# Kernel tuning notes

Measured on AMD Instinct MI355X. Metric: run time of the kernel, lower is better.

The kernel has to match this reference:

```python
import jax, jax.numpy as jnp
import numpy as np

B, H, VOCAB, STEPS = 256, 512, 100, 200  # TEXT_MAX_LEN - 1 = 200
SOS_IDX = 0  # char2idx['<SOS>'] == 0 (first entry of chars list)


def setup_inputs() -> dict:
    key = jax.random.key(0)
    ks = jax.random.split(key, 8)
    s = 0.05  # keep gates/tanh away from saturation, like trained-weight scale
    return {
        "feat": jax.random.normal(ks[0], (B, H), jnp.float32),          # resnet pooler_output
        "embed_table": jax.random.normal(ks[1], (VOCAB, H), jnp.float32) * s,
        "w_ih": jax.random.normal(ks[2], (3 * H, H), jnp.float32) * s,   # torch weight_ih_l0
        "w_hh": jax.random.normal(ks[3], (3 * H, H), jnp.float32) * s,   # torch weight_hh_l0
        "b_ih": jax.random.normal(ks[4], (3 * H,), jnp.float32) * s,
        "b_hh": jax.random.normal(ks[5], (3 * H,), jnp.float32) * s,
        "proj_w": jax.random.normal(ks[6], (VOCAB, H), jnp.float32) * s,
        "proj_b": jax.random.normal(ks[7], (VOCAB,), jnp.float32) * s,
    }


def _gru_cell(x, h, w_ih, w_hh, b_ih, b_hh):
    # torch GRU cell: gates ordered [r, z, n]
    gi = x @ w_ih.T + b_ih          # [B, 3H]
    gh = h @ w_hh.T + b_hh          # [B, 3H]
    i_r, i_z, i_n = jnp.split(gi, 3, axis=-1)
    h_r, h_z, h_n = jnp.split(gh, 3, axis=-1)
    r = jax.nn.sigmoid(i_r + h_r)
    z = jax.nn.sigmoid(i_z + h_z)
    n = jnp.tanh(i_n + r * h_n)
    return (1.0 - z) * n + z * h


def reference(feat, embed_table, w_ih, w_hh, b_ih, b_hh, proj_w, proj_b):
    batch = feat.shape[0]
    # hidden initialized from resnet features; first input = embed(<SOS>)
    h0 = feat                                             # [B, H]
    inp0 = jnp.broadcast_to(embed_table[SOS_IDX], (batch, H))

    def step(carry, _):
        inp, h = carry
        h_new = _gru_cell(inp, h, w_ih, w_hh, b_ih, b_hh)
        # GRU output == new hidden (1 layer); it is fed back as next input
        return (h_new, h_new), h_new

    _, outs = jax.lax.scan(step, (inp0, h0), None, length=STEPS)  # [T, B, H]
    res = jnp.transpose(outs, (1, 0, 2))                          # [B, T, H]
    logits = res @ proj_w.T + proj_b                              # [B, T, V]
    return jnp.transpose(logits, (0, 2, 1))                       # [B, V, T]
```

## Files before the change

### kernel.cpp

```cpp
#include <hip/hip_runtime.h>
#include <hip/hip_bf16.h>
#include <math.h>


typedef __bf16 bf16_t;
typedef __bf16 bf16x8 __attribute__((ext_vector_type(8)));
typedef float f32x4 __attribute__((ext_vector_type(4)));
typedef unsigned long long u64;
typedef unsigned short u16;

#define B_ 256
#define H_ 512
#define V_ 100
#define T_ 200
#define NF_ 131072
#define SLAB_ 24576
#define MFMA(a,b,c) __builtin_amdgcn_mfma_f32_16x16x32_bf16((a),(b),(c),0,0,0)

__device__ __forceinline__ float ld_in(const void* p, long i, int isf32) {
    return isf32 ? ((const float*)p)[i] : (float)((const bf16_t*)p)[i];
}

__device__ __forceinline__ bf16_t split_pick(double v, int sp) {
    bf16_t a = (bf16_t)(float)v;
    if (sp == 0) return a;
    double r1 = v - (double)(float)a;
    bf16_t b = (bf16_t)(float)r1;
    if (sp == 1) return b;
    double r2 = r1 - (double)(float)b;
    return (bf16_t)(float)r2;
}

union bfbits { __bf16 b; u16 u; };

__global__ __launch_bounds__(256) void convert_kernel(
    const void* __restrict__ feat, const void* __restrict__ embed,
    const void* __restrict__ wih,  const void* __restrict__ whh,
    const void* __restrict__ bih,  const void* __restrict__ bhh,
    const void* __restrict__ pw,   const void* __restrict__ pb,
    char* __restrict__ barr, int* __restrict__ flag,
    bf16_t* __restrict__ WB, bf16_t* __restrict__ W0, bf16_t* __restrict__ PB,
    bf16_t* __restrict__ hsp, double* __restrict__ hf,
    double* __restrict__ BB, double* __restrict__ pbd, double* __restrict__ gi0)
{
    __shared__ int s_cnt;
    if (threadIdx.x == 0) s_cnt = 0;
    __syncthreads();
    if (threadIdx.x < 128) {
        unsigned w = ((const unsigned*)feat)[threadIdx.x];
        unsigned e = (w >> 7) & 0xFFu;
        if (e >= 0x68u && e <= 0x85u) atomicAdd(&s_cnt, 1);
    }
    __syncthreads();
    const int isf32 = (s_cnt < 96) ? 1 : 0;
    if (blockIdx.x == 0) {
        if (threadIdx.x == 0) *flag = isf32;
        if (threadIdx.x < 48) {
            int i = threadIdx.x;
            int* p;
            if (i < 32)      p = (int*)(barr + (size_t)i * 128);
            else if (i < 40) p = (int*)(barr + 4096 + (size_t)(i - 32) * 128);
            else             p = (int*)(barr + 8192 + (size_t)(i - 40) * 128);
            *p = 0;
        }
    }

    const long S0 = NF_;
    const long S1 = 3145728;
    const long S2 = 2359296;
    const long S3 = 114688;
    const long S4 = 2048;
    const long S5 = 100;
    const long S6 = 1536;
    const long TOT = S0 + S1 + S2 + S3 + S4 + S5 + S6;

    for (long g = blockIdx.x * 256L + threadIdx.x; g < TOT;
         g += (long)gridDim.x * 256L) {
        long i = g;
        if (i < S0) {
            double v = (double)ld_in(feat, i, isf32);
            hf[i] = v;
            hsp[i] = split_pick(v, 0);
            hsp[NF_ + i] = split_pick(v, 1);
            hsp[2 * NF_ + i] = split_pick(v, 2);
            continue;
        }
        i -= S0;
        if (i < S1) {
            long slab = i / SLAB_;  long rem = i % SLAB_;
            int grp = (int)(slab >> 5), jt = (int)(slab & 31);
            int sp = (int)(rem / 8192); long r2 = rem % 8192;
            int c = (int)(r2 / 512), r = (int)((r2 % 512) / 32), kk = (int)(r2 & 31);
            long n = jt * 16 + r, k = c * 32 + kk;
            double v;
            if (grp == 0)      v = (double)ld_in(wih, n * H_ + k, isf32) +
                                   (double)ld_in(whh, n * H_ + k, isf32);
            else if (grp == 1) v = (double)ld_in(wih, (512 + n) * H_ + k, isf32) +
                                   (double)ld_in(whh, (512 + n) * H_ + k, isf32);
            else if (grp == 2) v = (double)ld_in(wih, (1024 + n) * H_ + k, isf32);
            else               v = (double)ld_in(whh, (1024 + n) * H_ + k, isf32);
            WB[i] = split_pick(v, sp);
            continue;
        }
        i -= S1;
        if (i < S2) {
            long slab = i / SLAB_;  long rem = i % SLAB_;
            int grp = (int)(slab >> 5), jt = (int)(slab & 31);
            int sp = (int)(rem / 8192); long r2 = rem % 8192;
            int c = (int)(r2 / 512), r = (int)((r2 % 512) / 32), kk = (int)(r2 & 31);
            long n = jt * 16 + r, k = c * 32 + kk;
            long row = (grp == 0) ? n : (grp == 1) ? (512 + n) : (1024 + n);
            W0[i] = split_pick((double)ld_in(whh, row * H_ + k, isf32), sp);
            continue;
        }
        i -= S2;
        if (i < S3) {
            int vt = (int)(i / 16384); long rem = i % 16384;
            int sp = (int)(rem / 8192); long r2 = rem % 8192;
            int c = (int)(r2 / 512), r = (int)((r2 % 512) / 32), kk = (int)(r2 & 31);
            int v = vt * 16 + r;
            long k = c * 32 + kk;
            double val = (v < V_) ? (double)ld_in(pw, (long)v * H_ + k, isf32) : 0.0;
            PB[i] = split_pick(val, sp);
            continue;
        }
        i -= S3;
        if (i < S4) {
            int grp = (int)(i / 512), j = (int)(i & 511);
            double v;
            if (grp == 0)      v = (double)ld_in(bih, j, isf32) + (double)ld_in(bhh, j, isf32);
            else if (grp == 1) v = (double)ld_in(bih, 512 + j, isf32) + (double)ld_in(bhh, 512 + j, isf32);
            else if (grp == 2) v = (double)ld_in(bih, 1024 + j, isf32);
            else               v = (double)ld_in(bhh, 1024 + j, isf32);
            BB[i] = v;
            continue;
        }
        i -= S4;
        if (i < S5) { pbd[i] = (double)ld_in(pb, i, isf32); continue; }
        i -= S5;
        if (i < S6) {
            double acc = 0.0;
            #pragma unroll 8
            for (int k = 0; k < H_; ++k)
                acc += (double)ld_in(embed, k, isf32) *
                       (double)ld_in(wih, i * H_ + k, isf32);
            gi0[i] = acc;
        }
    }
}

__global__ __launch_bounds__(512, 2) void gru_persist(
    const bf16_t* __restrict__ WB, const bf16_t* __restrict__ W0,
    const bf16_t* __restrict__ PB,
    bf16_t* __restrict__ hsp,
    const double* __restrict__ hf,
    const double* __restrict__ BB, const double* __restrict__ pbd,
    const double* __restrict__ gi0,
    const int* __restrict__ flag, char* __restrict__ barr,
    void* __restrict__ outp)
{
    __shared__ __align__(16) u64 Ad[2][3072];
    __shared__ double Gm[8][32][16];
    __shared__ __align__(16) bf16_t PBl[16384];

    const int tid = threadIdx.x;
    const int w = tid >> 6;
    const int g = w & 3;
    const int par = w >> 2;
    const int lane = tid & 63;
    const int ln = lane & 15;
    const int quad = lane >> 4;
    const int b = blockIdx.x;
    const int x = b & 7;
    const int l = b >> 3;
    const int jt = (x & 3) * 8 + (l & 7);
    const int mh = (x >> 2) * 4 + (l >> 3);
    const int m0base = mh * 32;
    const int isf32 = *flag;

    int* mysub = (int*)(barr + (size_t)(mh * 4 + (jt >> 3)) * 128);
    int* mytop = (int*)(barr + 4096 + (size_t)mh * 128);
    int* mys   = (int*)(barr + 8192 + (size_t)mh * 128);

    const int gm = tid >> 4;
    const int gj = tid & 15;
    const int jg = jt * 16 + gj;
    double hreg = hf[(long)(m0base + gm) * H_ + jg];
    const double bbR = BB[jg], bbZ = BB[512 + jg];
    const double bbNI = BB[1024 + jg], bbNH = BB[1536 + jg];
    const double g0R = gi0[jg], g0Z = gi0[512 + jg], g0NI = gi0[1024 + jg];

    bf16x8 Breg[8][3];
    {
        const int gg = (g == 3) ? 2 : g;
        const bf16_t* wpre = W0 + (long)(gg * 32 + jt) * SLAB_ + ln * 32 + quad * 8;
        #pragma unroll
        for (int n = 0; n < 8; ++n)
            #pragma unroll
            for (int sp = 0; sp < 3; ++sp)
                Breg[n][sp] = *(const bf16x8*)(wpre + sp * 8192 + (par + 2 * n) * 512);
    }
    const bf16_t* wpW = WB + (long)(g * 32 + jt) * SLAB_ + ln * 32 + quad * 8;

    const int tpj = jt & 1;

    if (jt < 14) {
        const bf16_t* src = PB + (long)(jt >> 1) * 16384;
        #pragma unroll
        for (int it = 0; it < 4; ++it) {
            int cg = it * 512 + tid;
            int h01 = cg >> 10, c = (cg >> 6) & 15, j = cg & 63;
            int L = (j & 3) * 16 + (j >> 2);
            *(bf16x8*)(PBl + h01 * 8192 + c * 512 + L * 8) =
                *(const bf16x8*)(src + cg * 8);
        }
    }

    const int lf = (((ln ^ quad) ^ ((ln & 1) << 2)) | (quad << 4)) * 8;

    int soff[6]; int ldst[6];
    #pragma unroll
    for (int i = 0; i < 6; ++i) {
        int u = i * 512 + tid;
        int sp = u >> 10, row = (u >> 5) & 31, k64 = u & 31;
        soff[i] = sp * 32768 + (m0base + row) * 128 + k64;
        int lc = k64 >> 3, qd = (k64 & 7) >> 1, half = k64 & 1;
        int lpos = (((row & 15) ^ qd) ^ ((row & 1) << 2)) | (qd << 4);
        ldst[i] = sp * 1024 + lc * 256 + (row >> 4) * 128 + lpos * 2 + half;
    }
    __syncthreads();

    for (int s = 0; s <= T_; ++s) {
        const u64* hin64 = (const u64*)(hsp + (long)(s & 1) * 3 * NF_);
        const bool gemm = (s < T_) && !(s == 0 && g == 2);
        const bool doproj = (s >= 1 && jt < 14 && w == (s & 7));

        double dg0[4] = {0, 0, 0, 0}, dg1[4] = {0, 0, 0, 0};
        f32x4 pacc = {0.f, 0.f, 0.f, 0.f};

        u64 sreg[24];
        #pragma unroll
        for (int qq = 0; qq < 4; ++qq)
            #pragma unroll
            for (int i = 0; i < 6; ++i)
                sreg[qq * 6 + i] = __hip_atomic_load(
                    hin64 + (long)soff[i] + qq * 32,
                    __ATOMIC_RELAXED, __HIP_MEMORY_SCOPE_AGENT);

        #pragma unroll
        for (int i = 0; i < 6; ++i) Ad[0][ldst[i]] = sreg[i];
        __syncthreads();

        #pragma unroll
        for (int q = 0; q < 4; ++q) {
            if (q < 3) {
                #pragma unroll
                for (int i = 0; i < 6; ++i)
                    Ad[(q + 1) & 1][ldst[i]] = sreg[(q + 1) * 6 + i];
            }
            const __bf16* Ab = (const __bf16*)(Ad[q & 1]);

            if (gemm) {
                #pragma unroll
                for (int t = 0; t < 2; ++t) {
                    const int lc = 2 * t + par;
                    const int n = 2 * q + t;
                    bf16x8 A0[3], A1[3];
                    #pragma unroll
                    for (int sp = 0; sp < 3; ++sp) {
                        A0[sp] = *(const bf16x8*)(Ab + sp * 4096 + lc * 1024 + lf);
                        A1[sp] = *(const bf16x8*)(Ab + sp * 4096 + lc * 1024 + 512 + lf);
                    }
                    f32x4 t0 = {0.f, 0.f, 0.f, 0.f};
                    t0 = MFMA(A0[0], Breg[n][2], t0);
                    t0 = MFMA(A0[1], Breg[n][1], t0);
                    t0 = MFMA(A0[2], Breg[n][0], t0);
                    t0 = MFMA(A0[0], Breg[n][1], t0);
                    t0 = MFMA(A0[1], Breg[n][0], t0);
                    t0 = MFMA(A0[0], Breg[n][0], t0);
                    f32x4 t1 = {0.f, 0.f, 0.f, 0.f};
                    t1 = MFMA(A1[0], Breg[n][2], t1);
                    t1 = MFMA(A1[1], Breg[n][1], t1);
                    t1 = MFMA(A1[2], Breg[n][0], t1);
                    t1 = MFMA(A1[0], Breg[n][1], t1);
                    t1 = MFMA(A1[1], Breg[n][0], t1);
                    t1 = MFMA(A1[0], Breg[n][0], t1);
                    #pragma unroll
                    for (int i = 0; i < 4; ++i) {
                        dg0[i] += (double)t0[i];
                        dg1[i] += (double)t1[i];
                    }
                }
            }
            if (doproj) {
                #pragma unroll
                for (int lc = 0; lc < 4; ++lc) {
                    const int c = q * 4 + lc;
                    bf16x8 pa1 = *(const bf16x8*)(Ab + 0 * 4096 + lc * 1024 + tpj * 512 + lf);
                    bf16x8 pa2 = *(const bf16x8*)(Ab + 1 * 4096 + lc * 1024 + tpj * 512 + lf);
                    bf16x8 b1v = *(const bf16x8*)(PBl + c * 512 + lane * 8);
                    bf16x8 b2v = *(const bf16x8*)(PBl + 8192 + c * 512 + lane * 8);
                    pacc = MFMA(pa1, b2v, pacc);
                    pacc = MFMA(pa2, b1v, pacc);
                    pacc = MFMA(pa1, b1v, pacc);
                }
            }
            if (q == 3 && s < T_) {
                #pragma unroll
                for (int i = 0; i < 4; ++i) {
                    Gm[w][quad * 4 + i][ln] = dg0[i];
                    Gm[w][16 + quad * 4 + i][ln] = dg1[i];
                }
            }
            __syncthreads();
        }

        if (doproj) {
            const int v = (jt >> 1) * 16 + ln;
            if (v < V_) {
                const double pbv = pbd[v];
                const int mtp = mh * 2 + tpj;
                #pragma unroll
                for (int i = 0; i < 4; ++i) {
                    const int m = mtp * 16 + quad * 4 + i;
                    const long idx = ((long)m * V_ + v) * T_ + (s - 1);
                    const float val = (float)((double)pacc[i] + pbv);
                    if (isf32) ((float*)outp)[idx] = val;
                    else       ((bf16_t*)outp)[idx] = (bf16_t)val;
                }
            }
        }

        if (s < T_) {
            {
                double R  = Gm[0][gm][gj] + Gm[4][gm][gj] + bbR;
                double Z  = Gm[1][gm][gj] + Gm[5][gm][gj] + bbZ;
                double NI = Gm[2][gm][gj] + Gm[6][gm][gj] + bbNI;
                double NH = Gm[3][gm][gj] + Gm[7][gm][gj] + bbNH;
                if (s == 0) { R += g0R; Z += g0Z; NI += g0NI; }
                const double r = 1.0 / (1.0 + exp(-R));
                const double z = 1.0 / (1.0 + exp(-Z));
                const double pre = NI + r * NH;
                const double n = 1.0 - 2.0 / (exp(2.0 * pre) + 1.0);
                hreg = (1.0 - z) * n + z * hreg;
                const long oi = (long)(m0base + gm) * H_ + jg;
                u16* ho = (u16*)(hsp + (long)((s + 1) & 1) * 3 * NF_);
                bfbits q1, q2, q3;
                q1.b = (bf16_t)(float)hreg;  double r1 = hreg - (double)(float)q1.b;
                q2.b = (bf16_t)(float)r1;    double r2 = r1 - (double)(float)q2.b;
                q3.b = (bf16_t)(float)r2;
                __hip_atomic_store(ho + oi, q1.u, __ATOMIC_RELAXED, __HIP_MEMORY_SCOPE_AGENT);
                __hip_atomic_store(ho + NF_ + oi, q2.u, __ATOMIC_RELAXED, __HIP_MEMORY_SCOPE_AGENT);
                __hip_atomic_store(ho + 2 * NF_ + oi, q3.u, __ATOMIC_RELAXED, __HIP_MEMORY_SCOPE_AGENT);
            }

            __syncthreads();
            if (tid == 0) {
                int old = __hip_atomic_fetch_add(mysub, 1, __ATOMIC_RELAXED,
                                                 __HIP_MEMORY_SCOPE_AGENT);
                if (old == 8 * (s + 1) - 1) {
                    int told = __hip_atomic_fetch_add(mytop, 1, __ATOMIC_RELAXED,
                                                      __HIP_MEMORY_SCOPE_AGENT);
                    if (told == 4 * (s + 1) - 1)
                        __hip_atomic_store(mys, s + 1, __ATOMIC_RELAXED,
                                           __HIP_MEMORY_SCOPE_AGENT);
                }
            }
            int lim = 0;
            while (__hip_atomic_load(mys, __ATOMIC_RELAXED,
                                     __HIP_MEMORY_SCOPE_AGENT) < s + 1) {
                __builtin_amdgcn_s_sleep(1);
                if (++lim > 100000000) break;
            }
            if (s == 0) {
                #pragma unroll
                for (int n = 0; n < 8; ++n)
                    #pragma unroll
                    for (int sp = 0; sp < 3; ++sp)
                        Breg[n][sp] = *(const bf16x8*)(wpW + sp * 8192 + (par + 2 * n) * 512);
            }
        }
    }
}

extern "C" void kernel_launch(void* const* d_in, const int* in_sizes, int n_in,
                              void* d_out, int out_size, void* d_ws, size_t ws_size,
                              hipStream_t stream) {
    char* ws = (char*)d_ws;
    char*   barr = ws;
    int*    flag = (int*)(ws + 16384);
    bf16_t* WB  = (bf16_t*)(ws + 16640);
    bf16_t* W0  = (bf16_t*)(ws + 6308096);
    bf16_t* PB  = (bf16_t*)(ws + 11026688);
    bf16_t* hsp = (bf16_t*)(ws + 11485440);
    double* hf  = (double*)(ws + 13058304);
    double* BB  = (double*)(ws + 14106880);
    double* pbd = (double*)(ws + 14123264);
    double* gi0 = (double*)(ws + 14124288);

    convert_kernel<<<1024, 256, 0, stream>>>(
        d_in[0], d_in[1], d_in[2], d_in[3], d_in[4], d_in[5], d_in[6], d_in[7],
        barr, flag, WB, W0, PB, hsp, hf, BB, pbd, gi0);

    gru_persist<<<256, 512, 0, stream>>>(
        WB, W0, PB, hsp, hf, BB, pbd, gi0, flag, barr, d_out);
}
```

Baseline: 1.555 ms.

## Map GRU blocks to XCCs at runtime and flatten per-group barrier

Each block reads its hardware XCC id and takes a slot from a per-XCC counter, so every batch group's 32 column tiles run on the same XCC and share its L2. The two-level sub/top barrier becomes a single flat counter per group. Only thread 0 spins, followed by a __syncthreads. The h-state exchange now uses plain stores and inline-asm sc0 loads with one explicit waitcnt. This relies on exactly 32 blocks landing on each XCC; any imbalance would give bad jt assignment or a hang. The relaxed memory semantics also depend on the XCC-local L2 being coherent.

```diff
diff --git a/kernel.cpp b/kernel.cpp
--- a/kernel.cpp
+++ b/kernel.cpp
@@ -55,13 +55,10 @@
     const int isf32 = (s_cnt < 96) ? 1 : 0;
     if (blockIdx.x == 0) {
         if (threadIdx.x == 0) *flag = isf32;
-        if (threadIdx.x < 48) {
-            int i = threadIdx.x;
-            int* p;
-            if (i < 32)      p = (int*)(barr + (size_t)i * 128);
-            else if (i < 40) p = (int*)(barr + 4096 + (size_t)(i - 32) * 128);
-            else             p = (int*)(barr + 8192 + (size_t)(i - 40) * 128);
-            *p = 0;
+        if (threadIdx.x < 24) {
+            int i = threadIdx.x & 7;
+            size_t base = (threadIdx.x < 8) ? 0 : (threadIdx.x < 16) ? 4096 : 8192;
+            *(int*)(barr + base + (size_t)i * 128) = 0;
         }
     }
 
@@ -162,6 +159,7 @@
     __shared__ __align__(16) u64 Ad[2][3072];
     __shared__ double Gm[8][32][16];
     __shared__ __align__(16) bf16_t PBl[16384];
+    __shared__ int s_slot;
 
     const int tid = threadIdx.x;
     const int w = tid >> 6;
@@ -170,17 +168,23 @@
     const int lane = tid & 63;
     const int ln = lane & 15;
     const int quad = lane >> 4;
-    const int b = blockIdx.x;
-    const int x = b & 7;
-    const int l = b >> 3;
-    const int jt = (x & 3) * 8 + (l & 7);
-    const int mh = (x >> 2) * 4 + (l >> 3);
+
+    unsigned xcc;
+    asm volatile("s_getreg_b32 %0, hwreg(HW_REG_XCC_ID)" : "=s"(xcc));
+    xcc &= 7u;
+    if (tid == 0) {
+        int* xslot = (int*)(barr + 8192 + (size_t)xcc * 128);
+        s_slot = __hip_atomic_fetch_add(xslot, 1, __ATOMIC_RELAXED,
+                                        __HIP_MEMORY_SCOPE_AGENT);
+    }
+    __syncthreads();
+    const int jt = s_slot & 31;
+    const int mh = (int)xcc;
     const int m0base = mh * 32;
     const int isf32 = *flag;
 
-    int* mysub = (int*)(barr + (size_t)(mh * 4 + (jt >> 3)) * 128);
-    int* mytop = (int*)(barr + 4096 + (size_t)mh * 128);
-    int* mys   = (int*)(barr + 8192 + (size_t)mh * 128);
+    int* myc = (int*)(barr + (size_t)mh * 128);
+    int* mys = (int*)(barr + 4096 + (size_t)mh * 128);
 
     const int gm = tid >> 4;
     const int gj = tid & 15;
@@ -242,10 +246,20 @@
         #pragma unroll
         for (int qq = 0; qq < 4; ++qq)
             #pragma unroll
-            for (int i = 0; i < 6; ++i)
-                sreg[qq * 6 + i] = __hip_atomic_load(
-                    hin64 + (long)soff[i] + qq * 32,
-                    __ATOMIC_RELAXED, __HIP_MEMORY_SCOPE_AGENT);
+            for (int i = 0; i < 6; ++i) {
+                const u64* p = hin64 + (long)soff[i] + qq * 32;
+                asm volatile("global_load_dwordx2 %0, %1, off sc0"
+                             : "=v"(sreg[qq * 6 + i]) : "v"(p));
+            }
+        asm volatile("s_waitcnt vmcnt(0)"
+            : "+v"(sreg[0]), "+v"(sreg[1]), "+v"(sreg[2]), "+v"(sreg[3]),
+              "+v"(sreg[4]), "+v"(sreg[5]), "+v"(sreg[6]), "+v"(sreg[7]),
+              "+v"(sreg[8]), "+v"(sreg[9]), "+v"(sreg[10]), "+v"(sreg[11]),
+              "+v"(sreg[12]), "+v"(sreg[13]), "+v"(sreg[14]), "+v"(sreg[15]),
+              "+v"(sreg[16]), "+v"(sreg[17]), "+v"(sreg[18]), "+v"(sreg[19]),
+              "+v"(sreg[20]), "+v"(sreg[21]), "+v"(sreg[22]), "+v"(sreg[23])
+            :: "memory");
+        __builtin_amdgcn_sched_barrier(0);
 
         #pragma unroll
         for (int i = 0; i < 6; ++i) Ad[0][ldst[i]] = sreg[i];
@@ -349,29 +363,26 @@
                 q1.b = (bf16_t)(float)hreg;  double r1 = hreg - (double)(float)q1.b;
                 q2.b = (bf16_t)(float)r1;    double r2 = r1 - (double)(float)q2.b;
                 q3.b = (bf16_t)(float)r2;
-                __hip_atomic_store(ho + oi, q1.u, __ATOMIC_RELAXED, __HIP_MEMORY_SCOPE_AGENT);
-                __hip_atomic_store(ho + NF_ + oi, q2.u, __ATOMIC_RELAXED, __HIP_MEMORY_SCOPE_AGENT);
-                __hip_atomic_store(ho + 2 * NF_ + oi, q3.u, __ATOMIC_RELAXED, __HIP_MEMORY_SCOPE_AGENT);
+                ho[oi] = q1.u;
+                ho[NF_ + oi] = q2.u;
+                ho[2 * NF_ + oi] = q3.u;
             }
 
             __syncthreads();
             if (tid == 0) {
-                int old = __hip_atomic_fetch_add(mysub, 1, __ATOMIC_RELAXED,
+                int old = __hip_atomic_fetch_add(myc, 1, __ATOMIC_RELAXED,
                                                  __HIP_MEMORY_SCOPE_AGENT);
-                if (old == 8 * (s + 1) - 1) {
-                    int told = __hip_atomic_fetch_add(mytop, 1, __ATOMIC_RELAXED,
-                                                      __HIP_MEMORY_SCOPE_AGENT);
-                    if (told == 4 * (s + 1) - 1)
-                        __hip_atomic_store(mys, s + 1, __ATOMIC_RELAXED,
-                                           __HIP_MEMORY_SCOPE_AGENT);
+                if (old == 32 * (s + 1) - 1)
+                    __hip_atomic_store(mys, s + 1, __ATOMIC_RELAXED,
+                                       __HIP_MEMORY_SCOPE_AGENT);
+                int lim = 0;
+                while (__hip_atomic_load(mys, __ATOMIC_RELAXED,
+                                         __HIP_MEMORY_SCOPE_AGENT) < s + 1) {
+                    __builtin_amdgcn_s_sleep(2);
+                    if (++lim > 100000000) break;
                 }
             }
-            int lim = 0;
-            while (__hip_atomic_load(mys, __ATOMIC_RELAXED,
-                                     __HIP_MEMORY_SCOPE_AGENT) < s + 1) {
-                __builtin_amdgcn_s_sleep(1);
-                if (++lim > 100000000) break;
-            }
+            __syncthreads();
             if (s == 0) {
                 #pragma unroll
                 for (int n = 0; n < 8; ++n)
```

New measurement: 1.530 ms. Within noise of the previous version (-1.6%).
